# Optimization experiments

Measured on AMD Instinct MI355X. Metric: run time of the kernel, lower is better.

Reference implementation:

```python
import jax, jax.numpy as jnp
import numpy as np

B, L, H, C = 1, 512, 1024, 2


def setup_inputs() -> dict:
    key = jax.random.key(0)
    k1, k2, k3 = jax.random.split(key, 3)
    lm_output = jax.random.normal(k1, (B, L, H), dtype=jnp.float32)
    # torch Linear weight layout: [out_features, in_features]
    W1 = jax.random.normal(k2, (H, 2 * H), dtype=jnp.float32) * 0.02
    b1 = jnp.zeros((H,), dtype=jnp.float32)
    W2 = jax.random.normal(k3, (C, H), dtype=jnp.float32) * 0.02
    b2 = jnp.zeros((C,), dtype=jnp.float32)
    return {"lm_output": lm_output, "W1": W1, "b1": b1, "W2": W2, "b2": b2}


def reference(lm_output, W1, b1, W2, b2):
    # pair_emb[b,i,j] = concat(lm_output[b,j], lm_output[b,i])
    # Linear(concat(a,b)) decomposes: split W1 into the halves acting on each part.
    Wa = W1[:, :H]  # acts on lm_output_a (the j / column token)
    Wb = W1[:, H:]  # acts on lm_output_b (the i / row token)
    a_proj = jnp.einsum('blh,oh->blo', lm_output, Wa)  # [B,L,H]
    b_proj = jnp.einsum('blh,oh->blo', lm_output, Wb)  # [B,L,H]
    # hidden[b,i,j] = tanh(a_proj[b,j] + b_proj[b,i] + b1)   -> [B,L,L,H]
    hidden = jnp.tanh(a_proj[:, None, :, :] + b_proj[:, :, None, :] + b1)
    # Dropout is identity at inference time.
    logits = jnp.einsum('bijh,ch->bijc', hidden, W2) + b2  # [B,L,L,C]
    logits = (logits + jnp.swapaxes(logits, 1, 2)) / 2.0
    return logits
```

## Files before the change

kernel.cpp:

```cpp
#include <hip/hip_runtime.h>
#include <hip/hip_bf16.h>

#define HH 1024
#define LL 512
#define NT 16
#define NTRI 136
#define NZ 8

typedef __attribute__((ext_vector_type(8))) short bf16x8;
typedef __attribute__((ext_vector_type(4))) float f32x4;

static constexpr float C_EXP = 2.8853900817779268f;

static __device__ __forceinline__ uint4 pack8(float4 a, float4 b) {
    union { uint4 u; __hip_bfloat162 h[4]; } r;
    r.h[0] = __float22bfloat162_rn(make_float2(a.x, a.y));
    r.h[1] = __float22bfloat162_rn(make_float2(a.z, a.w));
    r.h[2] = __float22bfloat162_rn(make_float2(b.x, b.y));
    r.h[3] = __float22bfloat162_rn(make_float2(b.z, b.w));
    return r.u;
}

__global__ __launch_bounds__(256) void convert_kernel(
    const float* __restrict__ lm, const float* __restrict__ W1,
    const float* __restrict__ W2,
    ushort* __restrict__ lm16, ushort* __restrict__ B16, float* __restrict__ wsum)
{
    const int b = blockIdx.x;
    if (b == 1280) {
        const int tid = threadIdx.x;
        if (tid < 128) {
            const int c = tid >> 6, l = tid & 63;
            float s = 0.f;
            for (int q = l; q < 256; q += 64) {
                const float4 v = *(const float4*)&W2[c * HH + q * 4];
                s += v.x + v.y + v.z + v.w;
            }
#pragma unroll
            for (int off = 32; off; off >>= 1) s += __shfl_down(s, off, 64);
            if (l == 0) wsum[c] = s;
        }
        return;
    }
    const int q = b * 256 + threadIdx.x;
    if (q < 65536) {
        const float4 a = *(const float4*)&lm[q * 8];
        const float4 c = *(const float4*)&lm[q * 8 + 4];
        ((uint4*)lm16)[q] = pack8(a, c);
    } else {
        const int p = q - 65536;
        const int n = p >> 7, k8 = (p & 127) * 8;
        const float* src = &W1[(n & 1023) * 2048 + (n >> 10) * 1024 + k8];
        ((uint4*)B16)[p] = pack8(*(const float4*)src, *(const float4*)(src + 4));
    }
}

__global__ __launch_bounds__(256, 4) void proj_mfma_kernel(
    const ushort* __restrict__ lm16, const ushort* __restrict__ B16,
    const float* __restrict__ b1, float* __restrict__ Ea, float* __restrict__ Eb)
{
    __shared__ ushort As[64][72];
    __shared__ ushort Bs[64][72];

    const int tid  = threadIdx.x;
    const int lane = tid & 63;
    const int w    = tid >> 6;
    const int b    = blockIdx.x;
    const int xcd  = b & 7;
    const int idx  = b >> 3;
    const int nbase = (xcd * 4 + (idx & 3)) * 64;
    const int mbase = (idx >> 2) * 64;
    const int wm   = w * 16;

    const int frow = lane & 15;
    const int q8   = (lane >> 4) * 8;

    f32x4 acc[4] = {};

    for (int kb = 0; kb < HH; kb += 64) {
        __syncthreads();
        {
            int p = tid;
#pragma unroll
            for (int it = 0; it < 2; ++it, p += 256) {
                const int row = p >> 3, c8 = (p & 7) * 8;
                *(uint4*)&As[row][c8] = *(const uint4*)&lm16[(mbase + row) * HH + kb + c8];
                *(uint4*)&Bs[row][c8] = *(const uint4*)&B16[(nbase + row) * HH + kb + c8];
            }
        }
        __syncthreads();

#pragma unroll
        for (int s = 0; s < 2; ++s) {
            const bf16x8 a = *(const bf16x8*)&As[wm + frow][s * 32 + q8];
#pragma unroll
            for (int nf = 0; nf < 4; ++nf) {
                const bf16x8 bb = *(const bf16x8*)&Bs[nf * 16 + frow][s * 32 + q8];
                acc[nf] = __builtin_amdgcn_mfma_f32_16x16x32_bf16(a, bb, acc[nf], 0, 0, 0);
            }
        }
    }

    const int col = lane & 15;
    const int rq  = (lane >> 4) * 4;
    const int m0  = mbase + wm + rq;
    const bool isA = nbase < HH;
#pragma unroll
    for (int nf = 0; nf < 4; ++nf) {
        const int nn = (nbase + nf * 16 + col) & 1023;
        if (isA) {
            const float bb = b1[nn];
#pragma unroll
            for (int r = 0; r < 4; ++r)
                Ea[(m0 + r) * HH + nn] = __builtin_amdgcn_exp2f(C_EXP * (acc[nf][r] + bb));
        } else {
#pragma unroll
            for (int r = 0; r < 4; ++r)
                Eb[(m0 + r) * HH + nn] = __builtin_amdgcn_exp2f(C_EXP * acc[nf][r]);
        }
    }
}

__global__ __launch_bounds__(256, 4) void pair_kernel(
    const float* __restrict__ Ea, const float* __restrict__ Eb,
    const float* __restrict__ W2, float* __restrict__ pbuf)
{
    __shared__ float eaj[32][68];
    __shared__ float eai[32][68];
    __shared__ float ebi[32][68];
    __shared__ float ebj[32][68];
    __shared__ float w0_s[128], w1_s[128];

    const int tid = threadIdx.x;
    const int tx  = tid & 15;
    const int ty  = tid >> 4;

    int tt = blockIdx.x, bi = 0, rem = NT;
    while (tt >= rem) { tt -= rem; --rem; ++bi; }
    const int bj    = bi + tt;
    const int ibase = bi * 32;
    const int jbase = bj * 32;
    const int slice = HH / NZ;
    const int k0    = blockIdx.y * slice;

    {
        if (tid < 64) {
            const int c = tid >= 32, q = tid - c * 32;
            ((float4*)(c ? w1_s : w0_s))[q] = *(const float4*)&W2[c * HH + k0 + q * 4];
        }
    }

    float acc[2][2][2] = {};

    for (int kb = 0; kb < slice; kb += 64) {
        __syncthreads();
        {
            int p = tid;
#pragma unroll
            for (int it = 0; it < 8; ++it, p += 256) {
                const int tile = p >> 9;
                const int row  = (p >> 4) & 31;
                const int c4   = p & 15;
                float4 v;
                if      (tile == 0) v = *(const float4*)&Ea[(jbase + row) * HH + k0 + kb + c4 * 4];
                else if (tile == 1) v = *(const float4*)&Ea[(ibase + row) * HH + k0 + kb + c4 * 4];
                else if (tile == 2) v = *(const float4*)&Eb[(ibase + row) * HH + k0 + kb + c4 * 4];
                else                v = *(const float4*)&Eb[(jbase + row) * HH + k0 + kb + c4 * 4];
                if      (tile == 0) *(float4*)&eaj[row][c4 * 4] = v;
                else if (tile == 1) *(float4*)&eai[row][c4 * 4] = v;
                else if (tile == 2) *(float4*)&ebi[row][c4 * 4] = v;
                else                *(float4*)&ebj[row][c4 * 4] = v;
            }
        }
        __syncthreads();

#pragma unroll 4
        for (int h4 = 0; h4 < 16; ++h4) {
            const float4 Aj0 = *(const float4*)&eaj[tx][h4 * 4];
            const float4 Aj1 = *(const float4*)&eaj[tx + 16][h4 * 4];
            const float4 Bi0 = *(const float4*)&ebi[ty][h4 * 4];
            const float4 Bi1 = *(const float4*)&ebi[ty + 16][h4 * 4];
            const float4 Ai0 = *(const float4*)&eai[ty][h4 * 4];
            const float4 Ai1 = *(const float4*)&eai[ty + 16][h4 * 4];
            const float4 Bj0 = *(const float4*)&ebj[tx][h4 * 4];
            const float4 Bj1 = *(const float4*)&ebj[tx + 16][h4 * 4];
            const float4 w0  = *(const float4*)&w0_s[kb + h4 * 4];
            const float4 w1  = *(const float4*)&w1_s[kb + h4 * 4];

#define DO_H(AJ0, AJ1, BI0, BI1, AI0, AI1, BJ0, BJ1, W0V, W1V)        \
            {                                                          \
                const float d00 = __builtin_fmaf((BI0), (AJ0), 1.f);   \
                const float d01 = __builtin_fmaf((BI0), (AJ1), 1.f);   \
                const float d10 = __builtin_fmaf((BI1), (AJ0), 1.f);   \
                const float d11 = __builtin_fmaf((BI1), (AJ1), 1.f);   \
                const float e00 = __builtin_fmaf((AI0), (BJ0), 1.f);   \
                const float e01 = __builtin_fmaf((AI0), (BJ1), 1.f);   \
                const float e10 = __builtin_fmaf((AI1), (BJ0), 1.f);   \
                const float e11 = __builtin_fmaf((AI1), (BJ1), 1.f);   \
                const float dp0 = d00 * d01, dp1 = d10 * d11;          \
                const float DR  = __builtin_amdgcn_rcpf(dp0 * dp1);    \
                const float dq0 = DR * dp1, dq1 = DR * dp0;            \
                const float rd00 = dq0 * d01, rd01 = dq0 * d00;        \
                const float rd10 = dq1 * d11, rd11 = dq1 * d10;        \
                const float ep0 = e00 * e01, ep1 = e10 * e11;          \
                const float ER  = __builtin_amdgcn_rcpf(ep0 * ep1);    \
                const float eq0 = ER * ep1, eq1 = ER * ep0;            \
                const float re00 = eq0 * e01, re01 = eq0 * e00;        \
                const float re10 = eq1 * e11, re11 = eq1 * e10;        \
                const float u00 = rd00 + re00, u01 = rd01 + re01;      \
                const float u10 = rd10 + re10, u11 = rd11 + re11;      \
                acc[0][0][0] = __builtin_fmaf(u00, (W0V), acc[0][0][0]); \
                acc[0][0][1] = __builtin_fmaf(u00, (W1V), acc[0][0][1]); \
                acc[0][1][0] = __builtin_fmaf(u01, (W0V), acc[0][1][0]); \
                acc[0][1][1] = __builtin_fmaf(u01, (W1V), acc[0][1][1]); \
                acc[1][0][0] = __builtin_fmaf(u10, (W0V), acc[1][0][0]); \
                acc[1][0][1] = __builtin_fmaf(u10, (W1V), acc[1][0][1]); \
                acc[1][1][0] = __builtin_fmaf(u11, (W0V), acc[1][1][0]); \
                acc[1][1][1] = __builtin_fmaf(u11, (W1V), acc[1][1][1]); \
            }
            DO_H(Aj0.x, Aj1.x, Bi0.x, Bi1.x, Ai0.x, Ai1.x, Bj0.x, Bj1.x, w0.x, w1.x)
            DO_H(Aj0.y, Aj1.y, Bi0.y, Bi1.y, Ai0.y, Ai1.y, Bj0.y, Bj1.y, w0.y, w1.y)
            DO_H(Aj0.z, Aj1.z, Bi0.z, Bi1.z, Ai0.z, Ai1.z, Bj0.z, Bj1.z, w0.z, w1.z)
            DO_H(Aj0.w, Aj1.w, Bi0.w, Bi1.w, Ai0.w, Ai1.w, Bj0.w, Bj1.w, w0.w, w1.w)
#undef DO_H
        }
    }

    float* pb = pbuf + ((size_t)blockIdx.y * NTRI + blockIdx.x) * 2048;
#pragma unroll
    for (int ii = 0; ii < 2; ++ii)
#pragma unroll
        for (int jj = 0; jj < 2; ++jj) {
            const int li = ty + ii * 16, lj = tx + jj * 16;
            *(float2*)&pb[(li * 32 + lj) * 2] =
                make_float2(acc[ii][jj][0], acc[ii][jj][1]);
        }
}

__global__ __launch_bounds__(256) void combine_kernel(
    const float* __restrict__ pbuf, const float* __restrict__ b2,
    const float* __restrict__ wsum, float* __restrict__ out)
{
    const int idx   = blockIdx.x * 256 + threadIdx.x;
    const int t     = idx >> 11;
    const int local = idx & 2047;
    int tt = t, bi = 0, rem = NT;
    while (tt >= rem) { tt -= rem; --rem; ++bi; }
    const int bj = bi + tt;

    float s = 0.f;
#pragma unroll
    for (int z = 0; z < NZ; ++z)
        s += pbuf[((size_t)z * NTRI + t) * 2048 + local];

    const int li = local >> 6;
    const int lj = (local >> 1) & 31;
    const int c  = local & 1;
    const float v = wsum[c] + b2[c] - s;

    const int i = bi * 32 + li;
    const int j = bj * 32 + lj;
    out[(i * LL + j) * 2 + c] = v;
    out[(j * LL + i) * 2 + c] = v;
}

extern "C" void kernel_launch(void* const* d_in, const int* in_sizes, int n_in,
                              void* d_out, int out_size, void* d_ws, size_t ws_size,
                              hipStream_t stream)
{
    const float* lm = (const float*)d_in[0];
    const float* W1 = (const float*)d_in[1];
    const float* b1 = (const float*)d_in[2];
    const float* W2 = (const float*)d_in[3];
    const float* b2 = (const float*)d_in[4];
    float* out = (float*)d_out;

    char* ws = (char*)d_ws;
    float*  Ea   = (float*)ws;
    float*  Eb   = (float*)(ws + (2u << 20));
    ushort* lm16 = (ushort*)(ws + (4u << 20));
    ushort* B16  = (ushort*)(ws + (5u << 20));
    float*  wsum = (float*)(ws + (9u << 20));
    float*  pbuf = (float*)(ws + (9u << 20) + 256);

    convert_kernel<<<1281, 256, 0, stream>>>(lm, W1, W2, lm16, B16, wsum);
    proj_mfma_kernel<<<256, 256, 0, stream>>>(lm16, B16, b1, Ea, Eb);
    pair_kernel<<<dim3(NTRI, NZ), 256, 0, stream>>>(Ea, Eb, W2, pbuf);
    combine_kernel<<<(NTRI * 2048) / 256, 256, 0, stream>>>(pbuf, b2, wsum, out);
}
```

Measured before the change: 135.6 us.

## Raise pair-kernel K-split, pack f32x2 math, deepen proj K tile, alias workspace

The pair kernel now splits the hidden dimension into 16 slices instead of 8 when the workspace is large enough, which doubles the grid for better CU occupancy. The price is more partial-sum traffic in the combine kernel, which now reads its slice count at runtime through two accumulators. The pair inner loop is rewritten with two-wide float vectors and interleaved W2 pairs so the compiler can emit packed FMA/MUL instructions. The projection GEMM stages 128-wide K tiles to halve barriers, and pbuf is aliased over the bf16 staging buffers to save workspace.

```diff
diff --git a/kernel.cpp b/kernel.cpp
--- a/kernel.cpp
+++ b/kernel.cpp
@@ -5,10 +5,10 @@
 #define LL 512
 #define NT 16
 #define NTRI 136
-#define NZ 8
 
 typedef __attribute__((ext_vector_type(8))) short bf16x8;
 typedef __attribute__((ext_vector_type(4))) float f32x4;
+typedef __attribute__((ext_vector_type(2))) float f32x2;
 
 static constexpr float C_EXP = 2.8853900817779268f;
 
@@ -59,8 +59,8 @@
     const ushort* __restrict__ lm16, const ushort* __restrict__ B16,
     const float* __restrict__ b1, float* __restrict__ Ea, float* __restrict__ Eb)
 {
-    __shared__ ushort As[64][72];
-    __shared__ ushort Bs[64][72];
+    __shared__ ushort As[64][136];
+    __shared__ ushort Bs[64][136];
 
     const int tid  = threadIdx.x;
     const int lane = tid & 63;
@@ -77,13 +77,13 @@
 
     f32x4 acc[4] = {};
 
-    for (int kb = 0; kb < HH; kb += 64) {
+    for (int kb = 0; kb < HH; kb += 128) {
         __syncthreads();
         {
             int p = tid;
 #pragma unroll
-            for (int it = 0; it < 2; ++it, p += 256) {
-                const int row = p >> 3, c8 = (p & 7) * 8;
+            for (int it = 0; it < 4; ++it, p += 256) {
+                const int row = p >> 4, c8 = (p & 15) * 8;
                 *(uint4*)&As[row][c8] = *(const uint4*)&lm16[(mbase + row) * HH + kb + c8];
                 *(uint4*)&Bs[row][c8] = *(const uint4*)&B16[(nbase + row) * HH + kb + c8];
             }
@@ -91,7 +91,7 @@
         __syncthreads();
 
 #pragma unroll
-        for (int s = 0; s < 2; ++s) {
+        for (int s = 0; s < 4; ++s) {
             const bf16x8 a = *(const bf16x8*)&As[wm + frow][s * 32 + q8];
 #pragma unroll
             for (int nf = 0; nf < 4; ++nf) {
@@ -123,13 +123,13 @@
 
 __global__ __launch_bounds__(256, 4) void pair_kernel(
     const float* __restrict__ Ea, const float* __restrict__ Eb,
-    const float* __restrict__ W2, float* __restrict__ pbuf)
+    const float* __restrict__ W2, float* __restrict__ pbuf, int slice)
 {
     __shared__ float eaj[32][68];
     __shared__ float eai[32][68];
     __shared__ float ebi[32][68];
     __shared__ float ebj[32][68];
-    __shared__ float w0_s[128], w1_s[128];
+    __shared__ f32x2 ws2[128];
 
     const int tid = threadIdx.x;
     const int tx  = tid & 15;
@@ -140,17 +140,13 @@
     const int bj    = bi + tt;
     const int ibase = bi * 32;
     const int jbase = bj * 32;
-    const int slice = HH / NZ;
     const int k0    = blockIdx.y * slice;
 
-    {
-        if (tid < 64) {
-            const int c = tid >= 32, q = tid - c * 32;
-            ((float4*)(c ? w1_s : w0_s))[q] = *(const float4*)&W2[c * HH + k0 + q * 4];
-        }
-    }
-
-    float acc[2][2][2] = {};
+    if (tid < slice)
+        ws2[tid] = (f32x2){W2[k0 + tid], W2[HH + k0 + tid]};
+
+    f32x2 acc2[2][2] = {};
+    const f32x2 one2 = {1.f, 1.f};
 
     for (int kb = 0; kb < slice; kb += 64) {
         __syncthreads();
@@ -184,44 +180,34 @@
             const float4 Ai1 = *(const float4*)&eai[ty + 16][h4 * 4];
             const float4 Bj0 = *(const float4*)&ebj[tx][h4 * 4];
             const float4 Bj1 = *(const float4*)&ebj[tx + 16][h4 * 4];
-            const float4 w0  = *(const float4*)&w0_s[kb + h4 * 4];
-            const float4 w1  = *(const float4*)&w1_s[kb + h4 * 4];
-
-#define DO_H(AJ0, AJ1, BI0, BI1, AI0, AI1, BJ0, BJ1, W0V, W1V)        \
-            {                                                          \
-                const float d00 = __builtin_fmaf((BI0), (AJ0), 1.f);   \
-                const float d01 = __builtin_fmaf((BI0), (AJ1), 1.f);   \
-                const float d10 = __builtin_fmaf((BI1), (AJ0), 1.f);   \
-                const float d11 = __builtin_fmaf((BI1), (AJ1), 1.f);   \
-                const float e00 = __builtin_fmaf((AI0), (BJ0), 1.f);   \
-                const float e01 = __builtin_fmaf((AI0), (BJ1), 1.f);   \
-                const float e10 = __builtin_fmaf((AI1), (BJ0), 1.f);   \
-                const float e11 = __builtin_fmaf((AI1), (BJ1), 1.f);   \
-                const float dp0 = d00 * d01, dp1 = d10 * d11;          \
-                const float DR  = __builtin_amdgcn_rcpf(dp0 * dp1);    \
-                const float dq0 = DR * dp1, dq1 = DR * dp0;            \
-                const float rd00 = dq0 * d01, rd01 = dq0 * d00;        \
-                const float rd10 = dq1 * d11, rd11 = dq1 * d10;        \
-                const float ep0 = e00 * e01, ep1 = e10 * e11;          \
-                const float ER  = __builtin_amdgcn_rcpf(ep0 * ep1);    \
-                const float eq0 = ER * ep1, eq1 = ER * ep0;            \
-                const float re00 = eq0 * e01, re01 = eq0 * e00;        \
-                const float re10 = eq1 * e11, re11 = eq1 * e10;        \
-                const float u00 = rd00 + re00, u01 = rd01 + re01;      \
-                const float u10 = rd10 + re10, u11 = rd11 + re11;      \
-                acc[0][0][0] = __builtin_fmaf(u00, (W0V), acc[0][0][0]); \
-                acc[0][0][1] = __builtin_fmaf(u00, (W1V), acc[0][0][1]); \
-                acc[0][1][0] = __builtin_fmaf(u01, (W0V), acc[0][1][0]); \
-                acc[0][1][1] = __builtin_fmaf(u01, (W1V), acc[0][1][1]); \
-                acc[1][0][0] = __builtin_fmaf(u10, (W0V), acc[1][0][0]); \
-                acc[1][0][1] = __builtin_fmaf(u10, (W1V), acc[1][0][1]); \
-                acc[1][1][0] = __builtin_fmaf(u11, (W0V), acc[1][1][0]); \
-                acc[1][1][1] = __builtin_fmaf(u11, (W1V), acc[1][1][1]); \
-            }
-            DO_H(Aj0.x, Aj1.x, Bi0.x, Bi1.x, Ai0.x, Ai1.x, Bj0.x, Bj1.x, w0.x, w1.x)
-            DO_H(Aj0.y, Aj1.y, Bi0.y, Bi1.y, Ai0.y, Ai1.y, Bj0.y, Bj1.y, w0.y, w1.y)
-            DO_H(Aj0.z, Aj1.z, Bi0.z, Bi1.z, Ai0.z, Ai1.z, Bj0.z, Bj1.z, w0.z, w1.z)
-            DO_H(Aj0.w, Aj1.w, Bi0.w, Bi1.w, Ai0.w, Ai1.w, Bj0.w, Bj1.w, w0.w, w1.w)
+            const f32x4 wA = *(const f32x4*)&ws2[kb + h4 * 4];
+            const f32x4 wB = *(const f32x4*)&ws2[kb + h4 * 4 + 2];
+
+#define DO_H(AJ0v, AJ1v, BI0v, BI1v, AI0v, AI1v, BJ0v, BJ1v, W01)            \
+            {                                                                 \
+                const f32x2 Aj = {AJ0v, AJ1v};                                \
+                const f32x2 Bj = {BJ0v, BJ1v};                                \
+                const f32x2 d0 = __builtin_elementwise_fma((f32x2){BI0v, BI0v}, Aj, one2); \
+                const f32x2 d1 = __builtin_elementwise_fma((f32x2){BI1v, BI1v}, Aj, one2); \
+                const f32x2 e0 = __builtin_elementwise_fma((f32x2){AI0v, AI0v}, Bj, one2); \
+                const f32x2 e1 = __builtin_elementwise_fma((f32x2){AI1v, AI1v}, Bj, one2); \
+                const float dp0 = d0.x * d0.y, dp1 = d1.x * d1.y;             \
+                const float ep0 = e0.x * e0.y, ep1 = e1.x * e1.y;             \
+                const float DR = __builtin_amdgcn_rcpf(dp0 * dp1);            \
+                const float ER = __builtin_amdgcn_rcpf(ep0 * ep1);            \
+                const f32x2 dq = (f32x2){DR, DR} * (f32x2){dp1, dp0};         \
+                const f32x2 eq = (f32x2){ER, ER} * (f32x2){ep1, ep0};         \
+                const f32x2 u0 = (f32x2){dq.x, dq.x} * d0.yx + (f32x2){eq.x, eq.x} * e0.yx; \
+                const f32x2 u1 = (f32x2){dq.y, dq.y} * d1.yx + (f32x2){eq.y, eq.y} * e1.yx; \
+                acc2[0][0] = __builtin_elementwise_fma((f32x2){u0.x, u0.x}, (W01), acc2[0][0]); \
+                acc2[0][1] = __builtin_elementwise_fma((f32x2){u0.y, u0.y}, (W01), acc2[0][1]); \
+                acc2[1][0] = __builtin_elementwise_fma((f32x2){u1.x, u1.x}, (W01), acc2[1][0]); \
+                acc2[1][1] = __builtin_elementwise_fma((f32x2){u1.y, u1.y}, (W01), acc2[1][1]); \
+            }
+            DO_H(Aj0.x, Aj1.x, Bi0.x, Bi1.x, Ai0.x, Ai1.x, Bj0.x, Bj1.x, wA.xy)
+            DO_H(Aj0.y, Aj1.y, Bi0.y, Bi1.y, Ai0.y, Ai1.y, Bj0.y, Bj1.y, wA.zw)
+            DO_H(Aj0.z, Aj1.z, Bi0.z, Bi1.z, Ai0.z, Ai1.z, Bj0.z, Bj1.z, wB.xy)
+            DO_H(Aj0.w, Aj1.w, Bi0.w, Bi1.w, Ai0.w, Ai1.w, Bj0.w, Bj1.w, wB.zw)
 #undef DO_H
         }
     }
@@ -232,14 +218,13 @@
 #pragma unroll
         for (int jj = 0; jj < 2; ++jj) {
             const int li = ty + ii * 16, lj = tx + jj * 16;
-            *(float2*)&pb[(li * 32 + lj) * 2] =
-                make_float2(acc[ii][jj][0], acc[ii][jj][1]);
+            *(f32x2*)&pb[(li * 32 + lj) * 2] = acc2[ii][jj];
         }
 }
 
 __global__ __launch_bounds__(256) void combine_kernel(
     const float* __restrict__ pbuf, const float* __restrict__ b2,
-    const float* __restrict__ wsum, float* __restrict__ out)
+    const float* __restrict__ wsum, float* __restrict__ out, int nz)
 {
     const int idx   = blockIdx.x * 256 + threadIdx.x;
     const int t     = idx >> 11;
@@ -248,10 +233,12 @@
     while (tt >= rem) { tt -= rem; --rem; ++bi; }
     const int bj = bi + tt;
 
-    float s = 0.f;
-#pragma unroll
-    for (int z = 0; z < NZ; ++z)
-        s += pbuf[((size_t)z * NTRI + t) * 2048 + local];
+    float s0 = 0.f, s1 = 0.f;
+    for (int z = 0; z < nz; z += 2) {
+        s0 += pbuf[((size_t)z * NTRI + t) * 2048 + local];
+        s1 += pbuf[((size_t)(z + 1) * NTRI + t) * 2048 + local];
+    }
+    const float s = s0 + s1;
 
     const int li = local >> 6;
     const int lj = (local >> 1) & 31;
@@ -278,13 +265,19 @@
     char* ws = (char*)d_ws;
     float*  Ea   = (float*)ws;
     float*  Eb   = (float*)(ws + (2u << 20));
-    ushort* lm16 = (ushort*)(ws + (4u << 20));
-    ushort* B16  = (ushort*)(ws + (5u << 20));
-    float*  wsum = (float*)(ws + (9u << 20));
-    float*  pbuf = (float*)(ws + (9u << 20) + 256);
+    float*  wsum = (float*)(ws + (4u << 20));
+    char*   ub   = ws + (4u << 20) + 256;
+    ushort* lm16 = (ushort*)ub;
+    ushort* B16  = (ushort*)(ub + (1u << 20));
+    float*  pbuf = (float*)ub;
+
+    const size_t ubase  = (4u << 20) + 256;
+    const size_t pb16   = (size_t)16 * NTRI * 2048 * 4;
+    const int nz = (ws_size >= ubase + pb16) ? 16 : 8;
+    const int slice = HH / nz;
 
     convert_kernel<<<1281, 256, 0, stream>>>(lm, W1, W2, lm16, B16, wsum);
     proj_mfma_kernel<<<256, 256, 0, stream>>>(lm16, B16, b1, Ea, Eb);
-    pair_kernel<<<dim3(NTRI, NZ), 256, 0, stream>>>(Ea, Eb, W2, pbuf);
-    combine_kernel<<<(NTRI * 2048) / 256, 256, 0, stream>>>(pbuf, b2, wsum, out);
-}
+    pair_kernel<<<dim3(NTRI, nz), 256, 0, stream>>>(Ea, Eb, W2, pbuf, slice);
+    combine_kernel<<<(NTRI * 2048) / 256, 256, 0, stream>>>(pbuf, b2, wsum, out, nz);
+}
```

After: 129.5 us. 1.05x faster.
